# Kernel optimization log

Hardware: AMD Instinct MI355X
Metric: run time of the kernel (lower is better)

## Reference

```python
import jax, jax.numpy as jnp
import numpy as np

B, S_PREV, E, H, LOW = 8, 4095, 2048, 16, 512
HD = E // H  # 128
ROPE_BASE = 10000.0


def _rope(x, pos):
    # x: [..., S, d], pos: [S]; half-split rotary
    d = x.shape[-1]
    half = d // 2
    inv_freq = 1.0 / (ROPE_BASE ** (jnp.arange(half, dtype=jnp.float32) / half))
    ang = pos.astype(jnp.float32)[:, None] * inv_freq  # [S, half]
    cos, sin = jnp.cos(ang), jnp.sin(ang)
    x1, x2 = x[..., :half], x[..., half:]
    return jnp.concatenate([x1 * cos - x2 * sin, x1 * sin + x2 * cos], axis=-1)


def setup_inputs() -> dict:
    key = jax.random.key(0)
    ks = jax.random.split(key, 10)

    def w(k, *shape):
        return jax.random.normal(k, shape, dtype=jnp.float32) * (1.0 / np.float32(np.sqrt(shape[0])))

    return {
        "x": jax.random.normal(ks[0], (B, 1, E), dtype=jnp.float32),
        "ckv_cache": jax.random.normal(ks[1], (B, S_PREV, LOW), dtype=jnp.float32),
        "kr_cache": jax.random.normal(ks[2], (B, S_PREV, HD), dtype=jnp.float32),
        "Wdq": w(ks[3], E, E),
        "Wuq": w(ks[4], E, E),
        "Wqr": w(ks[5], E, HD),
        "Wdkv": w(ks[6], E, LOW),
        "Wkr": w(ks[7], E, HD),
        "fused_upsample": w(ks[8], LOW, 2 * E),
        "Wo": w(ks[9], E, E),
    }


def reference(x, ckv_cache, kr_cache, Wdq, Wuq, Wqr, Wdkv, Wkr, fused_upsample, Wo):
    Bx = x.shape[0]
    # update compressed KV caches with the current token
    ckv = jnp.concatenate([ckv_cache, x @ Wdkv], axis=1)            # [B,S,LOW]
    kr = jnp.concatenate([kr_cache, x @ Wkr], axis=1)               # [B,S,HD]
    S = ckv.shape[1]
    up = ckv @ fused_upsample                                       # [B,S,2E]
    k_up, v = up[..., :E], up[..., E:]
    Kc = k_up.reshape(Bx, S, H, HD).transpose(0, 2, 1, 3)           # [B,H,S,HD]
    Kr = _rope(kr, jnp.arange(S))                                   # [B,S,HD] shared rope-K
    Kr = jnp.broadcast_to(Kr[:, None], (Bx, H, S, HD))
    v = v.reshape(Bx, S, H, HD).transpose(0, 2, 1, 3)               # [B,H,S,HD]
    # query path
    Cq = x @ Wdq                                                    # [B,1,E]
    Qc = (Cq @ Wuq).reshape(Bx, 1, H, HD).transpose(0, 2, 1, 3)     # [B,H,1,HD]
    Qr = _rope(Cq @ Wqr, jnp.arange(S - 1, S))                      # [B,1,HD] at last pos
    Qr = jnp.broadcast_to(Qr[:, None], (Bx, H, 1, HD))
    q = jnp.concatenate([Qc, Qr], axis=-1)                          # [B,H,1,2HD]
    k = jnp.concatenate([Kc, Kr], axis=-1)                          # [B,H,S,2HD]
    scores = jnp.einsum('bhqd,bhkd->bhqk', q, k) / np.float32(np.sqrt(2 * HD))
    attn = jax.nn.softmax(scores, axis=-1)
    o = jnp.einsum('bhqk,bhkd->bhqd', attn, v)                      # [B,H,1,HD]
    out = o.transpose(0, 2, 1, 3).reshape(Bx, 1, E) @ Wo            # [B,1,E]
    return out
```

## Files before the change

### kernel.cpp

```cpp
#include <hip/hip_runtime.h>
#include <hip/hip_bf16.h>

#define B_ 8
#define SPREV 4095
#define S_ 4096
#define E_ 2048
#define H_ 16
#define HD_ 128
#define LOW_ 512
#define NCH 64
#define CHK 64
#define L2INV 0.207620506f
#define CKV4_N 4193280
#define CKV4_H 2096640

typedef short s8v __attribute__((ext_vector_type(8)));
typedef float f4v __attribute__((ext_vector_type(4)));

__device__ __forceinline__ short f2bf_s(float f) {
  return (short)__bfloat16_as_ushort(__float2bfloat16(f));
}
__device__ __forceinline__ float bf2f(unsigned short h) {
  union { unsigned u; float f; } v; v.u = ((unsigned)h) << 16;
  return v.f;
}
__device__ __forceinline__ void sink_f4(f4v v) {
  asm volatile("" :: "v"(v[0]), "v"(v[1]), "v"(v[2]), "v"(v[3]));
}

__global__ __launch_bounds__(256) void init_kernel(float* __restrict__ ws_pre,
                                                   float* __restrict__ out) {
  int i = blockIdx.x * 256 + threadIdx.x;
  if (i < 55296) ws_pre[i] = 0.f;
  else if (i < 71680) out[i - 55296] = 0.f;
}

__global__ __launch_bounds__(128) void matvec8(
    const float* __restrict__ x, int K,
    const float* __restrict__ W0, int N0, float* __restrict__ o0,
    const float* __restrict__ W1, int N1, float* __restrict__ o1,
    const float* __restrict__ W2, int N2, float* __restrict__ o2,
    const float* __restrict__ pf4, int pf_base4, int pf_n4, int pf_nb)
{
  int cb = blockIdx.x;
  int nb0 = N0 >> 7, nb1 = N1 >> 7, nb2 = N2 >> 7;
  int nbsum = nb0 + nb1 + nb2;
  if (cb >= nbsum) {
    int seg = (cb - nbsum) * gridDim.y + blockIdx.y;
    int ftid = seg * 128 + threadIdx.x;
    const f4v* p4 = (const f4v*)pf4;
    for (int i = pf_base4 + ftid; i < pf_base4 + pf_n4; i += pf_nb * 128) {
      f4v v = p4[i]; sink_f4(v);
    }
    return;
  }
  const float* W; float* o; int N, colbase;
  if (cb < nb0)            { W = W0; o = o0; N = N0; colbase = cb << 7; }
  else if (cb < nb0 + nb1) { W = W1; o = o1; N = N1; colbase = (cb - nb0) << 7; }
  else                     { W = W2; o = o2; N = N2; colbase = (cb - nb0 - nb1) << 7; }
  int col = colbase + threadIdx.x;
  int k0 = blockIdx.y * 32;
  float acc[B_];
  #pragma unroll
  for (int b = 0; b < B_; ++b) acc[b] = 0.f;
  const float* Wp = W + (size_t)k0 * N + col;
  #pragma unroll 8
  for (int k = 0; k < 32; ++k) {
    float wv = Wp[(size_t)k * N];
    #pragma unroll
    for (int b = 0; b < B_; ++b)
      acc[b] = fmaf(x[b * K + k0 + k], wv, acc[b]);
  }
  #pragma unroll
  for (int b = 0; b < B_; ++b) atomicAdd(&o[b * N + col], acc[b]);
}

__global__ __launch_bounds__(256) void qeff_kernel(
    const float* __restrict__ Qc, const float* __restrict__ FU,
    unsigned short* __restrict__ qeff,
    const float* __restrict__ pf4, int pf_base4, int pf_n4)
{
  int bx = blockIdx.x, b = blockIdx.y, t = threadIdx.x;
  if (bx >= 64) {
    int seg = (bx - 64) * 8 + b;
    int ftid = seg * 256 + t;
    const f4v* p4 = (const f4v*)pf4;
    for (int i = pf_base4 + ftid; i < pf_base4 + pf_n4; i += 512 * 256) {
      f4v v = p4[i]; sink_f4(v);
    }
    return;
  }
  int h = bx >> 2, lq = bx & 3;
  int g = t >> 4, li = t & 15;
  __shared__ float qs[HD_];
  if (t < 128) qs[t] = Qc[b * E_ + h * HD_ + t];
  __syncthreads();
  f4v q0 = *(const f4v*)&qs[li * 8];
  f4v q1 = *(const f4v*)&qs[li * 8 + 4];
  #pragma unroll 2
  for (int p = 0; p < 8; ++p) {
    int l = lq * 128 + p * 16 + g;
    const f4v* w4 = (const f4v*)(FU + (size_t)l * (2 * E_) + h * HD_ + li * 8);
    f4v w0 = w4[0], w1 = w4[1];
    float a = w0[0]*q0[0] + w0[1]*q0[1] + w0[2]*q0[2] + w0[3]*q0[3]
            + w1[0]*q1[0] + w1[1]*q1[1] + w1[2]*q1[2] + w1[3]*q1[3];
    a += __shfl_xor(a, 1); a += __shfl_xor(a, 2);
    a += __shfl_xor(a, 4); a += __shfl_xor(a, 8);
    if (li == 0) qeff[(size_t)(b * H_ + h) * LOW_ + l] = (unsigned short)f2bf_s(a);
  }
}

__global__ __launch_bounds__(512) void attn_kernel(
    const float* __restrict__ ckv_cache, const float* __restrict__ ckv_new,
    const unsigned short* __restrict__ qeff,
    const float* __restrict__ kr_cache, const float* __restrict__ kr_new,
    const float* __restrict__ qr_pre,
    unsigned short* __restrict__ acc_part, float* __restrict__ m_part,
    float* __restrict__ l_part)
{
  int chunk = blockIdx.x, b = blockIdx.y;
  int tid = threadIdx.x;
  int w = tid >> 6, lane = tid & 63;
  int kg = lane >> 4, l16 = lane & 15;
  __shared__ float S_lds[2][16 * 64];
  __shared__ unsigned short P_lds[16 * 64];
  __shared__ float qr_sh[128];
  __shared__ float rope_lds[64];

  if (tid < 64) {
    float invf = exp2f(-L2INV * (float)tid);
    float x1 = qr_pre[b * HD_ + tid], x2 = qr_pre[b * HD_ + 64 + tid];
    float sn, cs; sincosf(4095.0f * invf, &sn, &cs);
    qr_sh[tid]      = x1 * cs - x2 * sn;
    qr_sh[64 + tid] = x1 * sn + x2 * cs;
  }
  __syncthreads();

  {
    int kh = w >> 2;
    int s_loc = (w & 3) * 16 + l16;
    int s = chunk * CHK + s_loc;
    const float* crow = (s == S_ - 1) ? (ckv_new + b * LOW_)
                                      : (ckv_cache + ((size_t)b * SPREV + s) * LOW_);
    f4v acc0 = {0.f, 0.f, 0.f, 0.f};
    f4v acc1 = {0.f, 0.f, 0.f, 0.f};
    const s8v* qf = (const s8v*)(qeff + (size_t)(b * H_ + l16) * LOW_);
    #pragma unroll
    for (int bt = 0; bt < 2; ++bt) {
      f4v c0_[4], c1_[4];
      s8v aq[4];
      #pragma unroll
      for (int u = 0; u < 4; ++u) {
        int kk = kh * 8 + bt * 4 + u;
        const float* cp = crow + kk * 32 + kg * 8;
        c0_[u] = *(const f4v*)cp;
        c1_[u] = *(const f4v*)(cp + 4);
        aq[u] = qf[kk * 4 + kg];
      }
      #pragma unroll
      for (int u = 0; u < 4; ++u) {
        s8v bv;
        bv[0]=f2bf_s(c0_[u][0]); bv[1]=f2bf_s(c0_[u][1]);
        bv[2]=f2bf_s(c0_[u][2]); bv[3]=f2bf_s(c0_[u][3]);
        bv[4]=f2bf_s(c1_[u][0]); bv[5]=f2bf_s(c1_[u][1]);
        bv[6]=f2bf_s(c1_[u][2]); bv[7]=f2bf_s(c1_[u][3]);
        if (u & 1)
          acc1 = __builtin_amdgcn_mfma_f32_16x16x32_bf16(aq[u], bv, acc1, 0, 0, 0);
        else
          acc0 = __builtin_amdgcn_mfma_f32_16x16x32_bf16(aq[u], bv, acc0, 0, 0, 0);
      }
    }
    #pragma unroll
    for (int r = 0; r < 4; ++r) {
      int h = kg * 4 + r;
      S_lds[kh][h * 64 + (s_loc ^ ((h & 7) << 2))] = acc0[r] + acc1[r];
    }
    if (w < 4) {
      const float* krp = (s == S_ - 1) ? (kr_new + b * HD_)
                                       : (kr_cache + ((size_t)b * SPREV + s) * HD_);
      float fs = (float)s;
      float rdot = 0.f;
      #pragma unroll
      for (int q = 0; q < 4; ++q) {
        int j = kg * 16 + q * 4;
        f4v x1 = *(const f4v*)&krp[j];
        f4v x2 = *(const f4v*)&krp[64 + j];
        f4v qa = *(const f4v*)&qr_sh[j];
        f4v qb = *(const f4v*)&qr_sh[64 + j];
        #pragma unroll
        for (int k2 = 0; k2 < 4; ++k2) {
          float invf = exp2f(-L2INV * (float)(j + k2));
          float sn, cs; sincosf(fs * invf, &sn, &cs);
          rdot += qa[k2] * (x1[k2] * cs - x2[k2] * sn)
                + qb[k2] * (x1[k2] * sn + x2[k2] * cs);
        }
      }
      rdot += __shfl_xor(rdot, 16);
      rdot += __shfl_xor(rdot, 32);
      if (kg == 0) rope_lds[s_loc] = rdot;
    }
  }
  __syncthreads();

  {
    int half = lane >> 5;
    int h = w * 2 + half;
    int sl = lane & 31;
    int s0 = sl * 2;
    int c2 = (h & 7) << 2;
    float v0 = (S_lds[0][h * 64 + (s0 ^ c2)] + S_lds[1][h * 64 + (s0 ^ c2)]
                + rope_lds[s0]) * 0.0625f;
    float v1 = (S_lds[0][h * 64 + ((s0 + 1) ^ c2)] + S_lds[1][h * 64 + ((s0 + 1) ^ c2)]
                + rope_lds[s0 + 1]) * 0.0625f;
    float m = fmaxf(v0, v1);
    m = fmaxf(m, __shfl_xor(m, 1));  m = fmaxf(m, __shfl_xor(m, 2));
    m = fmaxf(m, __shfl_xor(m, 4));  m = fmaxf(m, __shfl_xor(m, 8));
    m = fmaxf(m, __shfl_xor(m, 16));
    float e0 = expf(v0 - m), e1 = expf(v1 - m);
    float lsum = e0 + e1;
    lsum += __shfl_xor(lsum, 1);  lsum += __shfl_xor(lsum, 2);
    lsum += __shfl_xor(lsum, 4);  lsum += __shfl_xor(lsum, 8);
    lsum += __shfl_xor(lsum, 16);
    unsigned pk = (unsigned)(unsigned short)f2bf_s(e0) |
                  ((unsigned)(unsigned short)f2bf_s(e1) << 16);
    *(unsigned*)&P_lds[h * 64 + (s0 ^ ((h & 7) << 3))] = pk;
    if (sl == 0) {
      int idx = (b * NCH + chunk) * H_ + h;
      m_part[idx] = m;
      l_part[idx] = lsum;
    }
  }
  __syncthreads();

  {
    s8v pa[2];
    const float* rp[2][8];
    #pragma unroll
    for (int kt = 0; kt < 2; ++kt) {
      int so = kt * 32 + kg * 8;
      pa[kt] = *(const s8v*)&P_lds[l16 * 64 + (so ^ ((l16 & 7) << 3))];
      #pragma unroll
      for (int i = 0; i < 8; ++i) {
        int s = chunk * CHK + so + i;
        rp[kt][i] = (s == S_ - 1) ? (ckv_new + b * LOW_)
                                  : (ckv_cache + ((size_t)b * SPREV + s) * LOW_);
      }
    }
    f4v oa[4];
    #pragma unroll
    for (int nt = 0; nt < 4; ++nt) oa[nt] = {0.f, 0.f, 0.f, 0.f};
    #pragma unroll
    for (int nt = 0; nt < 4; ++nt) {
      int l = w * 64 + nt * 16 + l16;
      float vb0[8], vb1[8];
      #pragma unroll
      for (int i = 0; i < 8; ++i) { vb0[i] = rp[0][i][l]; vb1[i] = rp[1][i][l]; }
      s8v bv0, bv1;
      #pragma unroll
      for (int i = 0; i < 8; ++i) {
        bv0[i] = f2bf_s(vb0[i]);
        bv1[i] = f2bf_s(vb1[i]);
      }
      oa[nt] = __builtin_amdgcn_mfma_f32_16x16x32_bf16(pa[0], bv0, oa[nt], 0, 0, 0);
      oa[nt] = __builtin_amdgcn_mfma_f32_16x16x32_bf16(pa[1], bv1, oa[nt], 0, 0, 0);
    }
    size_t base = (size_t)(b * NCH + chunk) * H_;
    #pragma unroll
    for (int nt = 0; nt < 4; ++nt) {
      int l = w * 64 + nt * 16 + l16;
      #pragma unroll
      for (int r = 0; r < 4; ++r) {
        int h = kg * 4 + r;
        acc_part[(base + h) * LOW_ + l] = (unsigned short)f2bf_s(oa[nt][r]);
      }
    }
  }
}

__global__ __launch_bounds__(128) void reduce_proj_kernel(
    const float* __restrict__ m_part, const float* __restrict__ l_part,
    const unsigned short* __restrict__ acc_part, const float* __restrict__ FU,
    float* __restrict__ o_heads)
{
  int h = blockIdx.x, b = blockIdx.y, lz = blockIdx.z, t = threadIdx.x;
  __shared__ float wls[NCH];
  __shared__ float Linv_s;
  __shared__ float pa0[128], pa1[128];
  __shared__ float wl_sh[64];
  if (t < 64) {
    float mc = m_part[(b * NCH + t) * H_ + h];
    float M = mc;
    #pragma unroll
    for (int d = 1; d < 64; d <<= 1) M = fmaxf(M, __shfl_xor(M, d));
    float wc = expf(mc - M);
    float L = l_part[(b * NCH + t) * H_ + h] * wc;
    #pragma unroll
    for (int d = 1; d < 64; d <<= 1) L += __shfl_xor(L, d);
    wls[t] = wc;
    if (t == 0) Linv_s = 1.0f / L;
  }
  __syncthreads();
  {
    int p = t & 31, ch = t >> 5;
    int l0 = lz * 64 + p * 2;
    float a0 = 0.f, a1 = 0.f;
    const unsigned short* ap =
        acc_part + ((size_t)(b * NCH + ch * 16) * H_ + h) * LOW_ + l0;
    #pragma unroll 4
    for (int c = 0; c < 16; ++c) {
      unsigned pk = *(const unsigned*)(ap + (size_t)c * H_ * LOW_);
      float wc = wls[ch * 16 + c];
      a0 = fmaf(bf2f((unsigned short)(pk & 0xffffu)), wc, a0);
      a1 = fmaf(bf2f((unsigned short)(pk >> 16)),     wc, a1);
    }
    pa0[t] = a0; pa1[t] = a1;
  }
  __syncthreads();
  if (t < 32) {
    float inv = Linv_s;
    float s0 = pa0[t] + pa0[t + 32] + pa0[t + 64] + pa0[t + 96];
    float s1 = pa1[t] + pa1[t + 32] + pa1[t + 64] + pa1[t + 96];
    wl_sh[t * 2]     = s0 * inv;
    wl_sh[t * 2 + 1] = s1 * inv;
  }
  __syncthreads();
  {
    float a = 0.f;
    const float* fp = FU + (size_t)(lz * 64) * (2 * E_) + E_ + h * HD_ + t;
    #pragma unroll 4
    for (int l = 0; l < 64; ++l)
      a = fmaf(wl_sh[l], fp[(size_t)l * (2 * E_)], a);
    atomicAdd(&o_heads[(b * H_ + h) * HD_ + t], a);
  }
}

extern "C" void kernel_launch(void* const* d_in, const int* in_sizes, int n_in,
                              void* d_out, int out_size, void* d_ws, size_t ws_size,
                              hipStream_t stream)
{
  const float* x    = (const float*)d_in[0];
  const float* ckvc = (const float*)d_in[1];
  const float* krc  = (const float*)d_in[2];
  const float* Wdq  = (const float*)d_in[3];
  const float* Wuq  = (const float*)d_in[4];
  const float* Wqr  = (const float*)d_in[5];
  const float* Wdkv = (const float*)d_in[6];
  const float* Wkr  = (const float*)d_in[7];
  const float* FU   = (const float*)d_in[8];
  const float* Wo   = (const float*)d_in[9];
  float* out = (float*)d_out;

  char* ws = (char*)d_ws;
  float* Cq             = (float*)(ws + 0);
  float* Qc             = (float*)(ws + 65536);
  float* qr_pre         = (float*)(ws + 131072);
  float* ckvn           = (float*)(ws + 135168);
  float* krn            = (float*)(ws + 151552);
  float* o_heads        = (float*)(ws + 155648);
  unsigned short* qeff  = (unsigned short*)(ws + 221184);
  float* m_part         = (float*)(ws + 352256);
  float* l_part         = (float*)(ws + 385024);
  unsigned short* accp  = (unsigned short*)(ws + 417792);

  init_kernel<<<280, 256, 0, stream>>>((float*)ws, out);

  matvec8<<<dim3(21, 64), 128, 0, stream>>>(x, E_, Wdq, E_, Cq,
                                            Wdkv, LOW_, ckvn, Wkr, HD_, krn,
                                            (const float*)nullptr, 0, 0, 1);
  matvec8<<<dim3(34, 64), 128, 0, stream>>>(Cq, E_, Wuq, E_, Qc,
                                            Wqr, HD_, qr_pre,
                                            (const float*)nullptr, 0, (float*)nullptr,
                                            ckvc, 0, CKV4_H, 1088);
  qeff_kernel<<<dim3(128, 8), 256, 0, stream>>>(Qc, FU, qeff,
                                                ckvc, CKV4_H, CKV4_H);
  attn_kernel<<<dim3(64, 8), 512, 0, stream>>>(ckvc, ckvn, qeff, krc, krn,
                                               qr_pre, accp, m_part, l_part);
  reduce_proj_kernel<<<dim3(16, 8, 8), 128, 0, stream>>>(m_part, l_part, accp,
                                                         FU, o_heads);
  matvec8<<<dim3(16, 64), 128, 0, stream>>>(o_heads, E_, Wo, E_, out,
                                            (const float*)nullptr, 0, (float*)nullptr,
                                            (const float*)nullptr, 0, (float*)nullptr,
                                            (const float*)nullptr, 0, 0, 1);
}
```

Measured before the change: 85.97 us.

## Convert ckv cache to bf16 in side blocks and read bf16 in attention

The idle side blocks of the matvec and qeff kernels previously only prefetched the fp32 ckv cache into L2. They now convert it to bf16 and write it into a workspace buffer, along with the new token's row. The attention kernel then reads the bf16 copy directly, which halves its cache traffic and removes the per-element conversions in both MFMA phases. In exchange the earlier kernels pay an extra ~33 MB write, and attention may no longer hit the L2-warmed data.

```diff
diff --git a/kernel.cpp b/kernel.cpp
--- a/kernel.cpp
+++ b/kernel.cpp
@@ -11,8 +11,8 @@
 #define NCH 64
 #define CHK 64
 #define L2INV 0.207620506f
-#define CKV4_N 4193280
-#define CKV4_H 2096640
+#define CKV_CH 2096640
+#define CKV_CH_H 1048320
 
 typedef short s8v __attribute__((ext_vector_type(8)));
 typedef float f4v __attribute__((ext_vector_type(4)));
@@ -24,8 +24,13 @@
   union { unsigned u; float f; } v; v.u = ((unsigned)h) << 16;
   return v.f;
 }
-__device__ __forceinline__ void sink_f4(f4v v) {
-  asm volatile("" :: "v"(v[0]), "v"(v[1]), "v"(v[2]), "v"(v[3]));
+__device__ __forceinline__ void cvt8_store(const float* src, short* dst) {
+  f4v a0 = *(const f4v*)src;
+  f4v a1 = *(const f4v*)(src + 4);
+  s8v bv;
+  bv[0]=f2bf_s(a0[0]); bv[1]=f2bf_s(a0[1]); bv[2]=f2bf_s(a0[2]); bv[3]=f2bf_s(a0[3]);
+  bv[4]=f2bf_s(a1[0]); bv[5]=f2bf_s(a1[1]); bv[6]=f2bf_s(a1[2]); bv[7]=f2bf_s(a1[3]);
+  *(s8v*)dst = bv;
 }
 
 __global__ __launch_bounds__(256) void init_kernel(float* __restrict__ ws_pre,
@@ -40,7 +45,8 @@
     const float* __restrict__ W0, int N0, float* __restrict__ o0,
     const float* __restrict__ W1, int N1, float* __restrict__ o1,
     const float* __restrict__ W2, int N2, float* __restrict__ o2,
-    const float* __restrict__ pf4, int pf_base4, int pf_n4, int pf_nb)
+    const float* __restrict__ cf32, short* __restrict__ c16,
+    int cv_base, int cv_n, int cv_nb)
 {
   int cb = blockIdx.x;
   int nb0 = N0 >> 7, nb1 = N1 >> 7, nb2 = N2 >> 7;
@@ -48,10 +54,8 @@
   if (cb >= nbsum) {
     int seg = (cb - nbsum) * gridDim.y + blockIdx.y;
     int ftid = seg * 128 + threadIdx.x;
-    const f4v* p4 = (const f4v*)pf4;
-    for (int i = pf_base4 + ftid; i < pf_base4 + pf_n4; i += pf_nb * 128) {
-      f4v v = p4[i]; sink_f4(v);
-    }
+    for (int i = cv_base + ftid; i < cv_base + cv_n; i += cv_nb * 128)
+      cvt8_store(cf32 + (size_t)i * 8, c16 + (size_t)i * 8);
     return;
   }
   const float* W; float* o; int N, colbase;
@@ -78,16 +82,19 @@
 __global__ __launch_bounds__(256) void qeff_kernel(
     const float* __restrict__ Qc, const float* __restrict__ FU,
     unsigned short* __restrict__ qeff,
-    const float* __restrict__ pf4, int pf_base4, int pf_n4)
+    const float* __restrict__ cf32, short* __restrict__ c16,
+    const float* __restrict__ ckvn, short* __restrict__ ckvn16)
 {
   int bx = blockIdx.x, b = blockIdx.y, t = threadIdx.x;
   if (bx >= 64) {
     int seg = (bx - 64) * 8 + b;
+    if (seg == 0) {
+      cvt8_store(ckvn + (size_t)t * 8,        ckvn16 + (size_t)t * 8);
+      cvt8_store(ckvn + (size_t)(t + 256) * 8, ckvn16 + (size_t)(t + 256) * 8);
+    }
     int ftid = seg * 256 + t;
-    const f4v* p4 = (const f4v*)pf4;
-    for (int i = pf_base4 + ftid; i < pf_base4 + pf_n4; i += 512 * 256) {
-      f4v v = p4[i]; sink_f4(v);
-    }
+    for (int i = CKV_CH_H + ftid; i < CKV_CH; i += 512 * 256)
+      cvt8_store(cf32 + (size_t)i * 8, c16 + (size_t)i * 8);
     return;
   }
   int h = bx >> 2, lq = bx & 3;
@@ -111,7 +118,7 @@
 }
 
 __global__ __launch_bounds__(512) void attn_kernel(
-    const float* __restrict__ ckv_cache, const float* __restrict__ ckv_new,
+    const short* __restrict__ ckv16, const short* __restrict__ ckvn16,
     const unsigned short* __restrict__ qeff,
     const float* __restrict__ kr_cache, const float* __restrict__ kr_new,
     const float* __restrict__ qr_pre,
@@ -140,34 +147,26 @@
     int kh = w >> 2;
     int s_loc = (w & 3) * 16 + l16;
     int s = chunk * CHK + s_loc;
-    const float* crow = (s == S_ - 1) ? (ckv_new + b * LOW_)
-                                      : (ckv_cache + ((size_t)b * SPREV + s) * LOW_);
+    const short* crow = (s == S_ - 1) ? (ckvn16 + b * LOW_)
+                                      : (ckv16 + ((size_t)b * SPREV + s) * LOW_);
     f4v acc0 = {0.f, 0.f, 0.f, 0.f};
     f4v acc1 = {0.f, 0.f, 0.f, 0.f};
     const s8v* qf = (const s8v*)(qeff + (size_t)(b * H_ + l16) * LOW_);
     #pragma unroll
     for (int bt = 0; bt < 2; ++bt) {
-      f4v c0_[4], c1_[4];
-      s8v aq[4];
+      s8v bvv[4], aq[4];
       #pragma unroll
       for (int u = 0; u < 4; ++u) {
         int kk = kh * 8 + bt * 4 + u;
-        const float* cp = crow + kk * 32 + kg * 8;
-        c0_[u] = *(const f4v*)cp;
-        c1_[u] = *(const f4v*)(cp + 4);
-        aq[u] = qf[kk * 4 + kg];
+        bvv[u] = *(const s8v*)(crow + kk * 32 + kg * 8);
+        aq[u]  = qf[kk * 4 + kg];
       }
       #pragma unroll
       for (int u = 0; u < 4; ++u) {
-        s8v bv;
-        bv[0]=f2bf_s(c0_[u][0]); bv[1]=f2bf_s(c0_[u][1]);
-        bv[2]=f2bf_s(c0_[u][2]); bv[3]=f2bf_s(c0_[u][3]);
-        bv[4]=f2bf_s(c1_[u][0]); bv[5]=f2bf_s(c1_[u][1]);
-        bv[6]=f2bf_s(c1_[u][2]); bv[7]=f2bf_s(c1_[u][3]);
         if (u & 1)
-          acc1 = __builtin_amdgcn_mfma_f32_16x16x32_bf16(aq[u], bv, acc1, 0, 0, 0);
+          acc1 = __builtin_amdgcn_mfma_f32_16x16x32_bf16(aq[u], bvv[u], acc1, 0, 0, 0);
         else
-          acc0 = __builtin_amdgcn_mfma_f32_16x16x32_bf16(aq[u], bv, acc0, 0, 0, 0);
+          acc0 = __builtin_amdgcn_mfma_f32_16x16x32_bf16(aq[u], bvv[u], acc0, 0, 0, 0);
       }
     }
     #pragma unroll
@@ -234,7 +233,7 @@
 
   {
     s8v pa[2];
-    const float* rp[2][8];
+    const short* rp[2][8];
     #pragma unroll
     for (int kt = 0; kt < 2; ++kt) {
       int so = kt * 32 + kg * 8;
@@ -242,8 +241,8 @@
       #pragma unroll
       for (int i = 0; i < 8; ++i) {
         int s = chunk * CHK + so + i;
-        rp[kt][i] = (s == S_ - 1) ? (ckv_new + b * LOW_)
-                                  : (ckv_cache + ((size_t)b * SPREV + s) * LOW_);
+        rp[kt][i] = (s == S_ - 1) ? (ckvn16 + b * LOW_)
+                                  : (ckv16 + ((size_t)b * SPREV + s) * LOW_);
       }
     }
     f4v oa[4];
@@ -252,15 +251,9 @@
     #pragma unroll
     for (int nt = 0; nt < 4; ++nt) {
       int l = w * 64 + nt * 16 + l16;
-      float vb0[8], vb1[8];
-      #pragma unroll
-      for (int i = 0; i < 8; ++i) { vb0[i] = rp[0][i][l]; vb1[i] = rp[1][i][l]; }
       s8v bv0, bv1;
       #pragma unroll
-      for (int i = 0; i < 8; ++i) {
-        bv0[i] = f2bf_s(vb0[i]);
-        bv1[i] = f2bf_s(vb1[i]);
-      }
+      for (int i = 0; i < 8; ++i) { bv0[i] = rp[0][i][l]; bv1[i] = rp[1][i][l]; }
       oa[nt] = __builtin_amdgcn_mfma_f32_16x16x32_bf16(pa[0], bv0, oa[nt], 0, 0, 0);
       oa[nt] = __builtin_amdgcn_mfma_f32_16x16x32_bf16(pa[1], bv1, oa[nt], 0, 0, 0);
     }
@@ -361,24 +354,28 @@
   float* m_part         = (float*)(ws + 352256);
   float* l_part         = (float*)(ws + 385024);
   unsigned short* accp  = (unsigned short*)(ws + 417792);
+  short* ckv16          = (short*)(ws + 8806400);
+  short* ckvn16         = (short*)(ws + 42352640);
 
   init_kernel<<<280, 256, 0, stream>>>((float*)ws, out);
 
   matvec8<<<dim3(21, 64), 128, 0, stream>>>(x, E_, Wdq, E_, Cq,
                                             Wdkv, LOW_, ckvn, Wkr, HD_, krn,
-                                            (const float*)nullptr, 0, 0, 1);
+                                            (const float*)nullptr, (short*)nullptr,
+                                            0, 0, 1);
   matvec8<<<dim3(34, 64), 128, 0, stream>>>(Cq, E_, Wuq, E_, Qc,
                                             Wqr, HD_, qr_pre,
                                             (const float*)nullptr, 0, (float*)nullptr,
-                                            ckvc, 0, CKV4_H, 1088);
+                                            ckvc, ckv16, 0, CKV_CH_H, 1088);
   qeff_kernel<<<dim3(128, 8), 256, 0, stream>>>(Qc, FU, qeff,
-                                                ckvc, CKV4_H, CKV4_H);
-  attn_kernel<<<dim3(64, 8), 512, 0, stream>>>(ckvc, ckvn, qeff, krc, krn,
+                                                ckvc, ckv16, ckvn, ckvn16);
+  attn_kernel<<<dim3(64, 8), 512, 0, stream>>>(ckv16, ckvn16, qeff, krc, krn,
                                                qr_pre, accp, m_part, l_part);
   reduce_proj_kernel<<<dim3(16, 8, 8), 128, 0, stream>>>(m_part, l_part, accp,
                                                          FU, o_heads);
   matvec8<<<dim3(16, 64), 128, 0, stream>>>(o_heads, E_, Wo, E_, out,
                                             (const float*)nullptr, 0, (float*)nullptr,
                                             (const float*)nullptr, 0, (float*)nullptr,
-                                            (const float*)nullptr, 0, 0, 1);
-}
+                                            (const float*)nullptr, (short*)nullptr,
+                                            0, 0, 1);
+}
```

After: 84.82 us. About the same (-1.3%).
